# Kernel optimization log

Hardware: AMD Instinct MI355X
Metric: run time of the kernel (lower is better)

The kernel has to match this reference:

```python
import jax, jax.numpy as jnp
import numpy as np


def _gru(x, w_ih, w_hh, b_ih, b_hh):
    # x: [B, T, D]; torch nn.GRU (batch_first) semantics, h0 = 0
    B = x.shape[0]
    H = w_hh.shape[1]
    def step(h, xt):
        gi = xt @ w_ih.T + b_ih          # [B, 3H]
        gh = h @ w_hh.T + b_hh           # [B, 3H]
        ir, iz, inn = jnp.split(gi, 3, axis=-1)
        hr, hz, hn = jnp.split(gh, 3, axis=-1)
        r = jax.nn.sigmoid(ir + hr)
        z = jax.nn.sigmoid(iz + hz)
        n = jnp.tanh(inn + r * hn)
        h_new = (1.0 - z) * n + z * h
        return h_new, h_new
    h0 = jnp.zeros((B, H), x.dtype)
    _, ys = jax.lax.scan(step, h0, jnp.swapaxes(x, 0, 1))
    return jnp.swapaxes(ys, 0, 1)        # [B, T, H]


def setup_inputs() -> dict:
    key = jax.random.key(0)
    ks = iter(jax.random.split(key, 40))
    def p(shape, scale=0.05):
        return jax.random.normal(next(ks), shape, dtype=jnp.float32) * scale
    B, T, Z, S = 1024, 2, 100, 6
    return {
        "x": p((B, T, Z, S), 1.0),
        # actor: GRU(6 -> 64) + SimpleSubActor(64 -> 512 -> 128 -> 1)
        "a_gru_wih": p((192, 6)), "a_gru_whh": p((192, 64)),
        "a_gru_bih": p((192,)), "a_gru_bhh": p((192,)),
        "a_fc1_w": p((512, 64)), "a_fc1_b": p((512,)),
        "a_fc2_w": p((128, 512)), "a_fc2_b": p((128,)),
        "a_fc3_w": p((1, 128)), "a_fc3_b": p((1,)),
        # critic: GRU(35 -> 32) + SimpleSubCritic(32 -> 512 -> 256 -> 1)
        "c_gru_wih": p((96, 35)), "c_gru_whh": p((96, 32)),
        "c_gru_bih": p((96,)), "c_gru_bhh": p((96,)),
        "c_fc1_w": p((512, 32)), "c_fc1_b": p((512,)),
        "c_fc2_w": p((256, 512)), "c_fc2_b": p((256,)),
        "c_fc3_w": p((1, 256)), "c_fc3_b": p((1,)),
        # LocalizedModule(35 -> 512 -> 256 -> 1)
        "lm_fc1_w": p((512, 35)), "lm_fc1_b": p((512,)),
        "lm_fc2_w": p((256, 512)), "lm_fc2_b": p((256,)),
        "lm_fc3_w": p((1, 256)), "lm_fc3_b": p((1,)),
    }


def reference(x, a_gru_wih, a_gru_whh, a_gru_bih, a_gru_bhh,
              a_fc1_w, a_fc1_b, a_fc2_w, a_fc2_b, a_fc3_w, a_fc3_b,
              c_gru_wih, c_gru_whh, c_gru_bih, c_gru_bhh,
              c_fc1_w, c_fc1_b, c_fc2_w, c_fc2_b, c_fc3_w, c_fc3_b,
              lm_fc1_w, lm_fc1_b, lm_fc2_w, lm_fc2_b, lm_fc3_w, lm_fc3_b):
    B, T, Z, S = x.shape
    # ---- SimpleActor: same GRU+MLP shared across zones -> batch zones ----
    # torch: a[i] from x[:, :, i]; torch.stack(a) -> [Z, B, T, 1], then .view(-1, T, Z)
    xz = jnp.transpose(x, (2, 0, 1, 3)).reshape(Z * B, T, S)   # zones-major
    sx = _gru(xz, a_gru_wih, a_gru_whh, a_gru_bih, a_gru_bhh)  # [Z*B, T, 64]
    h = jax.nn.relu(sx @ a_fc1_w.T + a_fc1_b)
    h = jax.nn.relu(h @ a_fc2_w.T + a_fc2_b)
    sa = h @ a_fc3_w.T + a_fc3_b                               # [Z*B, T, 1]
    p = sa.reshape(-1, T, Z)                                   # faithful view(-1, t, nzones)
    # ---- concat action onto state ----
    xc = jnp.concatenate([x, p.reshape(-1, T, Z, 1)], axis=-1)  # [B, T, Z, 7]
    # ---- SimpleCritic: f/q lists reset each iter -> only zone i=99 survives ----
    # neighbors of 99: (99, 89, 100->zeros, 109->zeros, 98)
    zeros = jnp.zeros_like(xc[:, :, Z - 1])
    xi = jnp.concatenate([xc[:, :, 99], xc[:, :, 89], zeros, zeros, xc[:, :, 98]], axis=2)  # [B, T, 35]
    # LocalizedModule on last timestep
    hf = jax.nn.relu(xi[:, -1, :] @ lm_fc1_w.T + lm_fc1_b)
    hf = jax.nn.relu(hf @ lm_fc2_w.T + lm_fc2_b)
    f = hf @ lm_fc3_w.T + lm_fc3_b                             # [B, 1]
    # critic GRU + SimpleSubCritic (it keeps only last timestep)
    xq = _gru(xi, c_gru_wih, c_gru_whh, c_gru_bih, c_gru_bhh)  # [B, T, 32]
    hq = jax.nn.relu(xq[:, -1, :] @ c_fc1_w.T + c_fc1_b)
    hq = jax.nn.relu(hq @ c_fc2_w.T + c_fc2_b)
    qz = hq @ c_fc3_w.T + c_fc3_b                              # [B, 1]
    q = jnp.sum(f + qz, axis=1)                                # [B]
    return p[:, -1], q.reshape(-1, 1)
```

## Files before the change

### kernel.cpp

```cpp
#include <hip/hip_runtime.h>
#include <hip/hip_bf16.h>

#define NB 1024
#define NT 2
#define NZ 100
#define NS 6
#define NSEQ (NZ*NB)

typedef short short8 __attribute__((ext_vector_type(8)));
typedef float floatx4 __attribute__((ext_vector_type(4)));
typedef unsigned int uint2v __attribute__((ext_vector_type(2)));

__device__ __forceinline__ float sigm(float v)     { return 1.0f/(1.0f + __expf(-v)); }
__device__ __forceinline__ float tanhfast(float v) { float t = __expf(2.0f*v); return 1.0f - 2.0f/(t + 1.0f); }
__device__ __forceinline__ unsigned short f2bf(float f) {
    __hip_bfloat16 h = __float2bfloat16(f);
    return *reinterpret_cast<unsigned short*>(&h);
}

#define WS_WIHB   819200
#define WS_WHHB   (WS_WIHB + 192*32*2)
#define WS_W1B    (WS_WHHB + 192*64*2)
#define WS_W2B    (WS_W1B + 512*64*2)
#define WS_L1WB   (WS_W2B + 128*512*2)
#define WS_L2WB   (WS_L1WB + 512*64*2)
#define WS_CF1WB  (WS_L2WB + 256*512*2)
#define WS_CF2WB  (WS_CF1WB + 512*32*2)
#define WS_CWIHB  (WS_CF2WB + 256*512*2)
#define WS_CWHHB  (WS_CWIHB + 96*64*2)

#define PREP_N (116736 + 32768 + 131072 + 16384 + 131072 + 6144 + 3072)

__global__ __launch_bounds__(256)
void prep_kernel(const float* __restrict__ wih, const float* __restrict__ whh,
                 const float* __restrict__ w1,  const float* __restrict__ w2,
                 const float* __restrict__ l1w, const float* __restrict__ l2w,
                 const float* __restrict__ cf1w, const float* __restrict__ cf2w,
                 const float* __restrict__ cwih, const float* __restrict__ cwhh,
                 unsigned short* wihb, unsigned short* whhb,
                 unsigned short* w1b,  unsigned short* w2b,
                 unsigned short* l1wb, unsigned short* l2wb,
                 unsigned short* cf1wb, unsigned short* cf2wb,
                 unsigned short* cwihb, unsigned short* cwhhb)
{
    int e = blockIdx.x*256 + threadIdx.x;
    if (e < 6144) {
        int g = e >> 5, k = e & 31;
        wihb[e] = f2bf(k < 6 ? wih[g*6 + k] : 0.0f);
    } else if (e < 18432) {
        int i = e - 6144;  whhb[i] = f2bf(whh[i]);
    } else if (e < 51200) {
        int i = e - 18432; w1b[i] = f2bf(w1[i]);
    } else if (e < 116736) {
        int i = e - 51200; w2b[i] = f2bf(w2[i]);
    } else if (e < 149504) {
        int i = e - 116736; int o = i >> 6, k = i & 63;
        l1wb[i] = f2bf(k < 35 ? l1w[o*35 + k] : 0.0f);
    } else if (e < 280576) {
        int i = e - 149504; l2wb[i] = f2bf(l2w[i]);
    } else if (e < 296960) {
        int i = e - 280576; cf1wb[i] = f2bf(cf1w[i]);
    } else if (e < 428032) {
        int i = e - 296960; cf2wb[i] = f2bf(cf2w[i]);
    } else if (e < 434176) {
        int i = e - 428032; int o = i >> 6, k = i & 63;
        cwihb[i] = f2bf(k < 35 ? cwih[o*35 + k] : 0.0f);
    } else if (e < PREP_N) {
        int i = e - 434176; cwhhb[i] = f2bf(cwhh[i]);
    }
}

__device__ __forceinline__ int swz(int r) { return ((r & 7) << 4) | ((r & 8) << 3); }

__device__ __forceinline__ short8 ldsfrag(const char* base, int rowstride, int r, int k0) {
    int byte = r*rowstride + k0*2;
    byte ^= swz(r);
    return *reinterpret_cast<const short8*>(base + byte);
}

__device__ __forceinline__ short8 ldsfragC(const char* base, int rowstride, int r, int k0) {
    int byte = r*rowstride + k0*2;
    byte ^= ((r & 7) << 4);
    return *reinterpret_cast<const short8*>(base + byte);
}

__device__ __forceinline__ short8 xfrag(const float* __restrict__ xp) {
    float2 a  = *reinterpret_cast<const float2*>(xp);
    float2 b2 = *reinterpret_cast<const float2*>(xp + 2);
    float2 c  = *reinterpret_cast<const float2*>(xp + 4);
    short8 f;
    f[0] = (short)f2bf(a.x);  f[1] = (short)f2bf(a.y);
    f[2] = (short)f2bf(b2.x); f[3] = (short)f2bf(b2.y);
    f[4] = (short)f2bf(c.x);  f[5] = (short)f2bf(c.y);
    f[6] = 0; f[7] = 0;
    return f;
}

__global__ __launch_bounds__(256)
void actor_mfma(const float* __restrict__ x,
                const unsigned short* __restrict__ wihb, const unsigned short* __restrict__ whhb,
                const float* __restrict__ bih, const float* __restrict__ bhh,
                const unsigned short* __restrict__ w1b, const float* __restrict__ b1,
                const unsigned short* __restrict__ w2b, const float* __restrict__ b2,
                const float* __restrict__ w3, const float* __restrict__ b3,
                float* __restrict__ sa, float* __restrict__ out0)
{
    __shared__ __align__(16) char smem[24576];
    char*  sxb  = smem;
    float* fc3p = (float*)smem;
    char*  h1q  = smem + 8192;
    char*  h0b  = smem + 8192;

    const int tid  = threadIdx.x;
    const int wv   = tid >> 6;
    const int lane = tid & 63;
    const int r16  = lane & 15;
    const int g4   = lane >> 4;
    const int ft   = wv;
    const int s0   = blockIdx.x * 32;
    const int zz   = s0 >> 10;
    const int b0   = s0 & 1023;

    const int fb = ft*16 + g4*4;
    const floatx4 bihR = *reinterpret_cast<const floatx4*>(bih + fb);
    const floatx4 bihZ = *reinterpret_cast<const floatx4*>(bih + 64 + fb);
    const floatx4 bihN = *reinterpret_cast<const floatx4*>(bih + 128 + fb);
    const floatx4 bhhR = *reinterpret_cast<const floatx4*>(bhh + fb);
    const floatx4 bhhZ = *reinterpret_cast<const floatx4*>(bhh + 64 + fb);
    const floatx4 bhhN = *reinterpret_cast<const floatx4*>(bhh + 128 + fb);

    floatx4 h0v[2];
    floatx4 g1R[2], g1Z[2], g1N[2];

    {
        const short8 aR = *reinterpret_cast<const short8*>(wihb + ((ft     )*16 + r16)*32 + g4*8);
        const short8 aZ = *reinterpret_cast<const short8*>(wihb + ((ft +  4)*16 + r16)*32 + g4*8);
        const short8 aN = *reinterpret_cast<const short8*>(wihb + ((ft +  8)*16 + r16)*32 + g4*8);
        #pragma unroll
        for (int u = 0; u < 2; ++u) {
            const int seq = u*16 + r16;
            const float* xrow = x + (((b0 + seq)*NT)*NZ + zz)*NS;
            short8 bx0 = xfrag(xrow);
            short8 bx1 = xfrag(xrow + NZ*NS);
            floatx4 gR = {0,0,0,0}, gZ = {0,0,0,0}, gN = {0,0,0,0};
            gR = __builtin_amdgcn_mfma_f32_16x16x32_bf16(aR, bx0, gR, 0, 0, 0);
            gZ = __builtin_amdgcn_mfma_f32_16x16x32_bf16(aZ, bx0, gZ, 0, 0, 0);
            gN = __builtin_amdgcn_mfma_f32_16x16x32_bf16(aN, bx0, gN, 0, 0, 0);
            floatx4 tR = {0,0,0,0}, tZ = {0,0,0,0}, tN = {0,0,0,0};
            tR = __builtin_amdgcn_mfma_f32_16x16x32_bf16(aR, bx1, tR, 0, 0, 0);
            tZ = __builtin_amdgcn_mfma_f32_16x16x32_bf16(aZ, bx1, tZ, 0, 0, 0);
            tN = __builtin_amdgcn_mfma_f32_16x16x32_bf16(aN, bx1, tN, 0, 0, 0);
            g1R[u] = tR; g1Z[u] = tZ; g1N[u] = tN;
            floatx4 hh;
            #pragma unroll
            for (int q = 0; q < 4; ++q) {
                float r = sigm(gR[q] + bihR[q] + bhhR[q]);
                float z = sigm(gZ[q] + bihZ[q] + bhhZ[q]);
                float n = tanhfast(gN[q] + bihN[q] + r*bhhN[q]);
                hh[q] = (1.0f - z)*n;
            }
            h0v[u] = hh;
            unsigned int lo = (unsigned int)f2bf(hh[0]) | ((unsigned int)f2bf(hh[1]) << 16);
            unsigned int hi = (unsigned int)f2bf(hh[2]) | ((unsigned int)f2bf(hh[3]) << 16);
            uint2v vv = {lo, hi};
            int ba = seq*128 + fb*2; ba ^= swz(seq);
            *reinterpret_cast<uint2v*>(h0b + ba) = vv;
            *reinterpret_cast<uint2v*>(sxb + ba) = vv;
        }
    }
    __syncthreads();

    {
        const short8 wR0 = *reinterpret_cast<const short8*>(whhb + ((ft     )*16 + r16)*64 + g4*8);
        const short8 wR1 = *reinterpret_cast<const short8*>(whhb + ((ft     )*16 + r16)*64 + 32 + g4*8);
        const short8 wZ0 = *reinterpret_cast<const short8*>(whhb + ((ft +  4)*16 + r16)*64 + g4*8);
        const short8 wZ1 = *reinterpret_cast<const short8*>(whhb + ((ft +  4)*16 + r16)*64 + 32 + g4*8);
        const short8 wN0 = *reinterpret_cast<const short8*>(whhb + ((ft +  8)*16 + r16)*64 + g4*8);
        const short8 wN1 = *reinterpret_cast<const short8*>(whhb + ((ft +  8)*16 + r16)*64 + 32 + g4*8);
        #pragma unroll
        for (int u = 0; u < 2; ++u) {
            const int seq = u*16 + r16;
            short8 bh0 = ldsfrag(h0b, 128, seq, g4*8);
            short8 bh1 = ldsfrag(h0b, 128, seq, 32 + g4*8);
            floatx4 hR = {0,0,0,0}, hZ = {0,0,0,0}, hN = {0,0,0,0};
            hR = __builtin_amdgcn_mfma_f32_16x16x32_bf16(wR0, bh0, hR, 0, 0, 0);
            hZ = __builtin_amdgcn_mfma_f32_16x16x32_bf16(wZ0, bh0, hZ, 0, 0, 0);
            hN = __builtin_amdgcn_mfma_f32_16x16x32_bf16(wN0, bh0, hN, 0, 0, 0);
            hR = __builtin_amdgcn_mfma_f32_16x16x32_bf16(wR1, bh1, hR, 0, 0, 0);
            hZ = __builtin_amdgcn_mfma_f32_16x16x32_bf16(wZ1, bh1, hZ, 0, 0, 0);
            hN = __builtin_amdgcn_mfma_f32_16x16x32_bf16(wN1, bh1, hN, 0, 0, 0);
            floatx4 hn;
            #pragma unroll
            for (int q = 0; q < 4; ++q) {
                float r = sigm(g1R[u][q] + bihR[q] + hR[q] + bhhR[q]);
                float z = sigm(g1Z[u][q] + bihZ[q] + hZ[q] + bhhZ[q]);
                float n = tanhfast(g1N[u][q] + bihN[q] + r*(hN[q] + bhhN[q]));
                hn[q] = (1.0f - z)*n + z*h0v[u][q];
            }
            unsigned int lo = (unsigned int)f2bf(hn[0]) | ((unsigned int)f2bf(hn[1]) << 16);
            unsigned int hi = (unsigned int)f2bf(hn[2]) | ((unsigned int)f2bf(hn[3]) << 16);
            uint2v vv = {lo, hi};
            int row = 32 + seq;
            int ba = row*128 + fb*2; ba ^= swz(row);
            *reinterpret_cast<uint2v*>(sxb + ba) = vv;
        }
    }
    __syncthreads();

    const int mt0 = wv*2, mt1 = wv*2 + 1;
    floatx4 acc[2][4];
    {
        const floatx4 bA = *reinterpret_cast<const floatx4*>(b2 + mt0*16 + g4*4);
        const floatx4 bB = *reinterpret_cast<const floatx4*>(b2 + mt1*16 + g4*4);
        #pragma unroll
        for (int rt = 0; rt < 4; ++rt) { acc[0][rt] = bA; acc[1][rt] = bB; }
    }

    #pragma unroll
    for (int qq = 0; qq < 4; ++qq) {
        #pragma unroll
        for (int rt = 0; rt < 4; ++rt) {
            short8 f0 = ldsfrag(sxb, 128, rt*16 + r16, g4*8);
            short8 f1 = ldsfrag(sxb, 128, rt*16 + r16, 32 + g4*8);
            #pragma unroll
            for (int j = 0; j < 2; ++j) {
                int mtg = qq*8 + wv*2 + j;
                int mtl = wv*2 + j;
                const short8 a0 = *reinterpret_cast<const short8*>(w1b + (mtg*16 + r16)*64 + g4*8);
                const short8 a1 = *reinterpret_cast<const short8*>(w1b + (mtg*16 + r16)*64 + 32 + g4*8);
                floatx4 a = *reinterpret_cast<const floatx4*>(b1 + mtg*16 + g4*4);
                a = __builtin_amdgcn_mfma_f32_16x16x32_bf16(a0, f0, a, 0, 0, 0);
                a = __builtin_amdgcn_mfma_f32_16x16x32_bf16(a1, f1, a, 0, 0, 0);
                unsigned int lo = (unsigned int)f2bf(fmaxf(a[0],0.f)) | ((unsigned int)f2bf(fmaxf(a[1],0.f)) << 16);
                unsigned int hi = (unsigned int)f2bf(fmaxf(a[2],0.f)) | ((unsigned int)f2bf(fmaxf(a[3],0.f)) << 16);
                int row = rt*16 + r16;
                int byte = row*256 + (mtl*16 + g4*4)*2; byte ^= swz(row);
                uint2v vv = {lo, hi};
                *reinterpret_cast<uint2v*>(h1q + byte) = vv;
            }
        }
        __syncthreads();

        {
            const unsigned short* wp0 = w2b + (mt0*16 + r16)*512 + qq*128 + g4*8;
            const unsigned short* wp1 = w2b + (mt1*16 + r16)*512 + qq*128 + g4*8;
            #pragma unroll
            for (int ks = 0; ks < 4; ++ks) {
                const short8 a0 = *reinterpret_cast<const short8*>(wp0 + ks*32);
                const short8 a1 = *reinterpret_cast<const short8*>(wp1 + ks*32);
                #pragma unroll
                for (int rt = 0; rt < 4; ++rt) {
                    short8 bb = ldsfrag(h1q, 256, rt*16 + r16, ks*32 + g4*8);
                    acc[0][rt] = __builtin_amdgcn_mfma_f32_16x16x32_bf16(a0, bb, acc[0][rt], 0, 0, 0);
                    acc[1][rt] = __builtin_amdgcn_mfma_f32_16x16x32_bf16(a1, bb, acc[1][rt], 0, 0, 0);
                }
            }
        }
        __syncthreads();
    }

    {
        const floatx4 w3a = *reinterpret_cast<const floatx4*>(w3 + mt0*16 + g4*4);
        const floatx4 w3b = *reinterpret_cast<const floatx4*>(w3 + mt1*16 + g4*4);
        #pragma unroll
        for (int rt = 0; rt < 4; ++rt) {
            float p = fmaxf(acc[0][rt][0],0.f)*w3a[0] + fmaxf(acc[0][rt][1],0.f)*w3a[1]
                    + fmaxf(acc[0][rt][2],0.f)*w3a[2] + fmaxf(acc[0][rt][3],0.f)*w3a[3]
                    + fmaxf(acc[1][rt][0],0.f)*w3b[0] + fmaxf(acc[1][rt][1],0.f)*w3b[1]
                    + fmaxf(acc[1][rt][2],0.f)*w3b[2] + fmaxf(acc[1][rt][3],0.f)*w3b[3];
            p += __shfl_xor(p, 16);
            p += __shfl_xor(p, 32);
            if (g4 == 0) fc3p[wv*64 + rt*16 + r16] = p;
        }
    }
    __syncthreads();

    if (tid < 64) {
        float v = b3[0];
        #pragma unroll
        for (int w = 0; w < 4; ++w) v += fc3p[w*64 + tid];
        int t = tid >> 5, sl = tid & 31;
        int gseq = s0 + sl;
        int i = gseq*2 + t;
        sa[i] = v;
        int m = i % 200;
        if (m >= 100) out0[(i/200)*NZ + (m - 100)] = v;
    }
}

__global__ __launch_bounds__(512)
void critic_mfma(const float* __restrict__ x, const float* __restrict__ sa,
                 const unsigned short* __restrict__ cwihb, const unsigned short* __restrict__ cwhhb,
                 const float* __restrict__ cbih, const float* __restrict__ cbhh,
                 const unsigned short* __restrict__ cf1wb, const float* __restrict__ cf1b,
                 const unsigned short* __restrict__ cf2wb, const float* __restrict__ cf2b,
                 const float* __restrict__ cf3w, const float* __restrict__ cf3b,
                 const unsigned short* __restrict__ l1wb, const float* __restrict__ l1b,
                 const unsigned short* __restrict__ l2wb, const float* __restrict__ l2b,
                 const float* __restrict__ l3w, const float* __restrict__ l3b,
                 float* __restrict__ outq)
{
    __shared__ __align__(16) char smem[25600];
    char*  xib = smem;
    char*  h1b = smem + 4096;
    char*  h0b = smem + 20480;
    char*  hqb = smem + 22528;
    float* fp  = (float*)(smem + 24576);
    float* qp  = (float*)(smem + 25088);

    const int tid  = threadIdx.x;
    const int wv   = tid >> 6;
    const int lane = tid & 63;
    const int r16  = lane & 15;
    const int g4   = lane >> 4;
    const int b0   = blockIdx.x * 16;

    for (int e = tid; e < 2048; e += 512) {
        int trow = e >> 6, k = e & 63;
        int t = trow >> 4, row = trow & 15;
        int b = b0 + row;
        float v = 0.0f;
        if (k < 35) {
            int slot = k / 7, s = k - slot*7;
            int nb = (slot==0)?99:((slot==1)?89:((slot==4)?98:-1));
            if (nb >= 0) v = (s < 6) ? x[((b*NT + t)*NZ + nb)*NS + s]
                                     : sa[b*200 + t*100 + nb];
        }
        int byte = trow*128 + k*2; byte ^= ((trow & 7) << 4);
        *reinterpret_cast<unsigned short*>(xib + byte) = f2bf(v);
    }
    __syncthreads();

    {
        short8 bx0 = ldsfragC(xib, 128, 16 + r16, g4*8);
        short8 bx1 = ldsfragC(xib, 128, 16 + r16, 32 + g4*8);
        #pragma unroll
        for (int j = 0; j < 4; ++j) {
            int mt = wv*4 + j;
            const short8 a0 = *reinterpret_cast<const short8*>(l1wb + (mt*16 + r16)*64 + g4*8);
            const short8 a1 = *reinterpret_cast<const short8*>(l1wb + (mt*16 + r16)*64 + 32 + g4*8);
            floatx4 acc = *reinterpret_cast<const floatx4*>(l1b + mt*16 + g4*4);
            acc = __builtin_amdgcn_mfma_f32_16x16x32_bf16(a0, bx0, acc, 0, 0, 0);
            acc = __builtin_amdgcn_mfma_f32_16x16x32_bf16(a1, bx1, acc, 0, 0, 0);
            unsigned int lo = (unsigned int)f2bf(fmaxf(acc[0],0.f)) | ((unsigned int)f2bf(fmaxf(acc[1],0.f)) << 16);
            unsigned int hi = (unsigned int)f2bf(fmaxf(acc[2],0.f)) | ((unsigned int)f2bf(fmaxf(acc[3],0.f)) << 16);
            int byte = r16*1024 + (mt*16 + g4*4)*2; byte ^= ((r16 & 7) << 4);
            uint2v vv = {lo, hi};
            *reinterpret_cast<uint2v*>(h1b + byte) = vv;
        }
    }
    __syncthreads();

    {
        int mt0 = wv*2, mt1 = wv*2 + 1;
        floatx4 acc0 = *reinterpret_cast<const floatx4*>(l2b + mt0*16 + g4*4);
        floatx4 acc1 = *reinterpret_cast<const floatx4*>(l2b + mt1*16 + g4*4);
        const unsigned short* wp0 = l2wb + (mt0*16 + r16)*512 + g4*8;
        const unsigned short* wp1 = l2wb + (mt1*16 + r16)*512 + g4*8;
        for (int ks = 0; ks < 16; ++ks) {
            short8 bb = ldsfragC(h1b, 1024, r16, ks*32 + g4*8);
            const short8 a0 = *reinterpret_cast<const short8*>(wp0 + ks*32);
            const short8 a1 = *reinterpret_cast<const short8*>(wp1 + ks*32);
            acc0 = __builtin_amdgcn_mfma_f32_16x16x32_bf16(a0, bb, acc0, 0, 0, 0);
            acc1 = __builtin_amdgcn_mfma_f32_16x16x32_bf16(a1, bb, acc1, 0, 0, 0);
        }
        const floatx4 w0 = *reinterpret_cast<const floatx4*>(l3w + mt0*16 + g4*4);
        const floatx4 w1 = *reinterpret_cast<const floatx4*>(l3w + mt1*16 + g4*4);
        float p = fmaxf(acc0[0],0.f)*w0[0] + fmaxf(acc0[1],0.f)*w0[1]
                + fmaxf(acc0[2],0.f)*w0[2] + fmaxf(acc0[3],0.f)*w0[3]
                + fmaxf(acc1[0],0.f)*w1[0] + fmaxf(acc1[1],0.f)*w1[1]
                + fmaxf(acc1[2],0.f)*w1[2] + fmaxf(acc1[3],0.f)*w1[3];
        p += __shfl_xor(p, 16);
        p += __shfl_xor(p, 32);
        if (g4 == 0) fp[wv*16 + r16] = p;
    }
    __syncthreads();

    floatx4 h0r = {0,0,0,0};
    floatx4 gR1 = {0,0,0,0}, gZ1 = {0,0,0,0}, gN1 = {0,0,0,0};
    floatx4 bihR, bihZ, bihN, bhhR, bhhZ, bhhN;
    if (wv < 2) {
        const int hf = wv;
        const int fb = hf*16 + g4*4;
        bihR = *reinterpret_cast<const floatx4*>(cbih + fb);
        bihZ = *reinterpret_cast<const floatx4*>(cbih + 32 + fb);
        bihN = *reinterpret_cast<const floatx4*>(cbih + 64 + fb);
        bhhR = *reinterpret_cast<const floatx4*>(cbhh + fb);
        bhhZ = *reinterpret_cast<const floatx4*>(cbhh + 32 + fb);
        bhhN = *reinterpret_cast<const floatx4*>(cbhh + 64 + fb);
        short8 bx0 = ldsfragC(xib, 128, r16, g4*8);
        short8 bx1 = ldsfragC(xib, 128, r16, 32 + g4*8);
        short8 cx0 = ldsfragC(xib, 128, 16 + r16, g4*8);
        short8 cx1 = ldsfragC(xib, 128, 16 + r16, 32 + g4*8);
        floatx4 gR0 = {0,0,0,0}, gZ0 = {0,0,0,0}, gN0 = {0,0,0,0};
        #pragma unroll
        for (int p = 0; p < 2; ++p) {
            const short8 aR = *reinterpret_cast<const short8*>(cwihb + ((hf    )*16 + r16)*64 + p*32 + g4*8);
            const short8 aZ = *reinterpret_cast<const short8*>(cwihb + ((2+hf  )*16 + r16)*64 + p*32 + g4*8);
            const short8 aN = *reinterpret_cast<const short8*>(cwihb + ((4+hf  )*16 + r16)*64 + p*32 + g4*8);
            short8 b0f = p ? bx1 : bx0;
            short8 b1f = p ? cx1 : cx0;
            gR0 = __builtin_amdgcn_mfma_f32_16x16x32_bf16(aR, b0f, gR0, 0, 0, 0);
            gZ0 = __builtin_amdgcn_mfma_f32_16x16x32_bf16(aZ, b0f, gZ0, 0, 0, 0);
            gN0 = __builtin_amdgcn_mfma_f32_16x16x32_bf16(aN, b0f, gN0, 0, 0, 0);
            gR1 = __builtin_amdgcn_mfma_f32_16x16x32_bf16(aR, b1f, gR1, 0, 0, 0);
            gZ1 = __builtin_amdgcn_mfma_f32_16x16x32_bf16(aZ, b1f, gZ1, 0, 0, 0);
            gN1 = __builtin_amdgcn_mfma_f32_16x16x32_bf16(aN, b1f, gN1, 0, 0, 0);
        }
        #pragma unroll
        for (int q = 0; q < 4; ++q) {
            float r = sigm(gR0[q] + bihR[q] + bhhR[q]);
            float z = sigm(gZ0[q] + bihZ[q] + bhhZ[q]);
            float n = tanhfast(gN0[q] + bihN[q] + r*bhhN[q]);
            h0r[q] = (1.0f - z)*n;
        }
        unsigned int lo = (unsigned int)f2bf(h0r[0]) | ((unsigned int)f2bf(h0r[1]) << 16);
        unsigned int hi = (unsigned int)f2bf(h0r[2]) | ((unsigned int)f2bf(h0r[3]) << 16);
        uint2v vv = {lo, hi};
        int byte = r16*128 + fb*2; byte ^= ((r16 & 7) << 4);
        *reinterpret_cast<uint2v*>(h0b + byte) = vv;
    }
    __syncthreads();
    if (wv < 2) {
        const int hf = wv;
        const int fb = hf*16 + g4*4;
        short8 bh = ldsfragC(h0b, 128, r16, g4*8);
        const short8 aR = *reinterpret_cast<const short8*>(cwhhb + ((hf    )*16 + r16)*32 + g4*8);
        const short8 aZ = *reinterpret_cast<const short8*>(cwhhb + ((2+hf  )*16 + r16)*32 + g4*8);
        const short8 aN = *reinterpret_cast<const short8*>(cwhhb + ((4+hf  )*16 + r16)*32 + g4*8);
        floatx4 hR = {0,0,0,0}, hZ = {0,0,0,0}, hN = {0,0,0,0};
        hR = __builtin_amdgcn_mfma_f32_16x16x32_bf16(aR, bh, hR, 0, 0, 0);
        hZ = __builtin_amdgcn_mfma_f32_16x16x32_bf16(aZ, bh, hZ, 0, 0, 0);
        hN = __builtin_amdgcn_mfma_f32_16x16x32_bf16(aN, bh, hN, 0, 0, 0);
        floatx4 hn;
        #pragma unroll
        for (int q = 0; q < 4; ++q) {
            float r = sigm(gR1[q] + bihR[q] + hR[q] + bhhR[q]);
            float z = sigm(gZ1[q] + bihZ[q] + hZ[q] + bhhZ[q]);
            float n = tanhfast(gN1[q] + bihN[q] + r*(hN[q] + bhhN[q]));
            hn[q] = (1.0f - z)*n + z*h0r[q];
        }
        unsigned int lo = (unsigned int)f2bf(hn[0]) | ((unsigned int)f2bf(hn[1]) << 16);
        unsigned int hi = (unsigned int)f2bf(hn[2]) | ((unsigned int)f2bf(hn[3]) << 16);
        uint2v vv = {lo, hi};
        int byte = r16*128 + fb*2; byte ^= ((r16 & 7) << 4);
        *reinterpret_cast<uint2v*>(hqb + byte) = vv;
    }
    __syncthreads();

    {
        short8 bq = ldsfragC(hqb, 128, r16, g4*8);
        #pragma unroll
        for (int j = 0; j < 4; ++j) {
            int mt = wv*4 + j;
            const short8 a = *reinterpret_cast<const short8*>(cf1wb + (mt*16 + r16)*32 + g4*8);
            floatx4 acc = *reinterpret_cast<const floatx4*>(cf1b + mt*16 + g4*4);
            acc = __builtin_amdgcn_mfma_f32_16x16x32_bf16(a, bq, acc, 0, 0, 0);
            unsigned int lo = (unsigned int)f2bf(fmaxf(acc[0],0.f)) | ((unsigned int)f2bf(fmaxf(acc[1],0.f)) << 16);
            unsigned int hi = (unsigned int)f2bf(fmaxf(acc[2],0.f)) | ((unsigned int)f2bf(fmaxf(acc[3],0.f)) << 16);
            int byte = r16*1024 + (mt*16 + g4*4)*2; byte ^= ((r16 & 7) << 4);
            uint2v vv = {lo, hi};
            *reinterpret_cast<uint2v*>(h1b + byte) = vv;
        }
    }
    __syncthreads();

    {
        int mt0 = wv*2, mt1 = wv*2 + 1;
        floatx4 acc0 = *reinterpret_cast<const floatx4*>(cf2b + mt0*16 + g4*4);
        floatx4 acc1 = *reinterpret_cast<const floatx4*>(cf2b + mt1*16 + g4*4);
        const unsigned short* wp0 = cf2wb + (mt0*16 + r16)*512 + g4*8;
        const unsigned short* wp1 = cf2wb + (mt1*16 + r16)*512 + g4*8;
        for (int ks = 0; ks < 16; ++ks) {
            short8 bb = ldsfragC(h1b, 1024, r16, ks*32 + g4*8);
            const short8 a0 = *reinterpret_cast<const short8*>(wp0 + ks*32);
            const short8 a1 = *reinterpret_cast<const short8*>(wp1 + ks*32);
            acc0 = __builtin_amdgcn_mfma_f32_16x16x32_bf16(a0, bb, acc0, 0, 0, 0);
            acc1 = __builtin_amdgcn_mfma_f32_16x16x32_bf16(a1, bb, acc1, 0, 0, 0);
        }
        const floatx4 w0 = *reinterpret_cast<const floatx4*>(cf3w + mt0*16 + g4*4);
        const floatx4 w1 = *reinterpret_cast<const floatx4*>(cf3w + mt1*16 + g4*4);
        float p = fmaxf(acc0[0],0.f)*w0[0] + fmaxf(acc0[1],0.f)*w0[1]
                + fmaxf(acc0[2],0.f)*w0[2] + fmaxf(acc0[3],0.f)*w0[3]
                + fmaxf(acc1[0],0.f)*w1[0] + fmaxf(acc1[1],0.f)*w1[1]
                + fmaxf(acc1[2],0.f)*w1[2] + fmaxf(acc1[3],0.f)*w1[3];
        p += __shfl_xor(p, 16);
        p += __shfl_xor(p, 32);
        if (g4 == 0) qp[wv*16 + r16] = p;
    }
    __syncthreads();

    if (tid < 16) {
        float f = l3b[0], qz = cf3b[0];
        #pragma unroll
        for (int w = 0; w < 8; ++w) { f += fp[w*16 + tid]; qz += qp[w*16 + tid]; }
        outq[b0 + tid] = f + qz;
    }
}

extern "C" void kernel_launch(void* const* d_in, const int* in_sizes, int n_in,
                              void* d_out, int out_size, void* d_ws, size_t ws_size,
                              hipStream_t stream)
{
    (void)in_sizes; (void)n_in; (void)out_size; (void)ws_size;
    const float* x     = (const float*)d_in[0];
    const float* a_wih = (const float*)d_in[1];
    const float* a_whh = (const float*)d_in[2];
    const float* a_bih = (const float*)d_in[3];
    const float* a_bhh = (const float*)d_in[4];
    const float* a1w   = (const float*)d_in[5];
    const float* a1b   = (const float*)d_in[6];
    const float* a2w   = (const float*)d_in[7];
    const float* a2b   = (const float*)d_in[8];
    const float* a3w   = (const float*)d_in[9];
    const float* a3b   = (const float*)d_in[10];
    const float* cwih  = (const float*)d_in[11];
    const float* cwhh  = (const float*)d_in[12];
    const float* cbih  = (const float*)d_in[13];
    const float* cbhh  = (const float*)d_in[14];
    const float* cf1w  = (const float*)d_in[15];
    const float* cf1b  = (const float*)d_in[16];
    const float* cf2w  = (const float*)d_in[17];
    const float* cf2b  = (const float*)d_in[18];
    const float* cf3w  = (const float*)d_in[19];
    const float* cf3b  = (const float*)d_in[20];
    const float* l1w   = (const float*)d_in[21];
    const float* l1b   = (const float*)d_in[22];
    const float* l2w   = (const float*)d_in[23];
    const float* l2b   = (const float*)d_in[24];
    const float* l3w   = (const float*)d_in[25];
    const float* l3b   = (const float*)d_in[26];

    float* sa = (float*)d_ws;
    unsigned short* wihb  = (unsigned short*)((char*)d_ws + WS_WIHB);
    unsigned short* whhb  = (unsigned short*)((char*)d_ws + WS_WHHB);
    unsigned short* w1b   = (unsigned short*)((char*)d_ws + WS_W1B);
    unsigned short* w2b   = (unsigned short*)((char*)d_ws + WS_W2B);
    unsigned short* l1wb  = (unsigned short*)((char*)d_ws + WS_L1WB);
    unsigned short* l2wb  = (unsigned short*)((char*)d_ws + WS_L2WB);
    unsigned short* cf1wb = (unsigned short*)((char*)d_ws + WS_CF1WB);
    unsigned short* cf2wb = (unsigned short*)((char*)d_ws + WS_CF2WB);
    unsigned short* cwihb = (unsigned short*)((char*)d_ws + WS_CWIHB);
    unsigned short* cwhhb = (unsigned short*)((char*)d_ws + WS_CWHHB);
    float* out0 = (float*)d_out;
    float* outq = (float*)d_out + NB*NZ;

    hipLaunchKernelGGL(prep_kernel, dim3((PREP_N + 255)/256), dim3(256), 0, stream,
                       a_wih, a_whh, a1w, a2w, l1w, l2w, cf1w, cf2w, cwih, cwhh,
                       wihb, whhb, w1b, w2b, l1wb, l2wb, cf1wb, cf2wb, cwihb, cwhhb);
    hipLaunchKernelGGL(actor_mfma, dim3(NSEQ/32), dim3(256), 0, stream,
                       x, wihb, whhb, a_bih, a_bhh, w1b, a1b, w2b, a2b, a3w, a3b, sa, out0);
    hipLaunchKernelGGL(critic_mfma, dim3(NB/16), dim3(512), 0, stream,
                       x, sa, cwihb, cwhhb, cbih, cbhh, cf1wb, cf1b, cf2wb, cf2b, cf3w, cf3b,
                       l1wb, l1b, l2wb, l2b, l3w, l3b, outq);
}
```

Measured before the change: 153.0 us.

## Process actor fc1/fc2 in two 256-wide chunks and hoist LDS input fragments

The actor MLP's hidden layer was processed in four 128-wide chunks, each needing its own barrier. It now uses two 256-wide chunks in a larger shared buffer, which halves the barriers and drops the last one. The GRU-output fragments are loaded from shared memory once into registers instead of once per chunk. The redundant copy of h0 is removed by reading it from the shared sequence buffer, and the swizzle is simplified to one variant. In exchange, the kernel uses more shared memory and registers, which may lower occupancy.

```diff
diff --git a/kernel.cpp b/kernel.cpp
--- a/kernel.cpp
+++ b/kernel.cpp
@@ -70,17 +70,11 @@
     }
 }
 
-__device__ __forceinline__ int swz(int r) { return ((r & 7) << 4) | ((r & 8) << 3); }
+__device__ __forceinline__ int swz(int r) { return (r & 7) << 4; }
 
 __device__ __forceinline__ short8 ldsfrag(const char* base, int rowstride, int r, int k0) {
     int byte = r*rowstride + k0*2;
     byte ^= swz(r);
-    return *reinterpret_cast<const short8*>(base + byte);
-}
-
-__device__ __forceinline__ short8 ldsfragC(const char* base, int rowstride, int r, int k0) {
-    int byte = r*rowstride + k0*2;
-    byte ^= ((r & 7) << 4);
     return *reinterpret_cast<const short8*>(base + byte);
 }
 
@@ -105,11 +99,10 @@
                 const float* __restrict__ w3, const float* __restrict__ b3,
                 float* __restrict__ sa, float* __restrict__ out0)
 {
-    __shared__ __align__(16) char smem[24576];
+    __shared__ __align__(16) char smem[40960];
     char*  sxb  = smem;
     float* fc3p = (float*)smem;
-    char*  h1q  = smem + 8192;
-    char*  h0b  = smem + 8192;
+    char*  h1b  = smem + 8192;
 
     const int tid  = threadIdx.x;
     const int wv   = tid >> 6;
@@ -164,7 +157,6 @@
             unsigned int hi = (unsigned int)f2bf(hh[2]) | ((unsigned int)f2bf(hh[3]) << 16);
             uint2v vv = {lo, hi};
             int ba = seq*128 + fb*2; ba ^= swz(seq);
-            *reinterpret_cast<uint2v*>(h0b + ba) = vv;
             *reinterpret_cast<uint2v*>(sxb + ba) = vv;
         }
     }
@@ -180,8 +172,8 @@
         #pragma unroll
         for (int u = 0; u < 2; ++u) {
             const int seq = u*16 + r16;
-            short8 bh0 = ldsfrag(h0b, 128, seq, g4*8);
-            short8 bh1 = ldsfrag(h0b, 128, seq, 32 + g4*8);
+            short8 bh0 = ldsfrag(sxb, 128, seq, g4*8);
+            short8 bh1 = ldsfrag(sxb, 128, seq, 32 + g4*8);
             floatx4 hR = {0,0,0,0}, hZ = {0,0,0,0}, hN = {0,0,0,0};
             hR = __builtin_amdgcn_mfma_f32_16x16x32_bf16(wR0, bh0, hR, 0, 0, 0);
             hZ = __builtin_amdgcn_mfma_f32_16x16x32_bf16(wZ0, bh0, hZ, 0, 0, 0);
@@ -207,6 +199,13 @@
     }
     __syncthreads();
 
+    short8 fr[4][2];
+    #pragma unroll
+    for (int rt = 0; rt < 4; ++rt) {
+        fr[rt][0] = ldsfrag(sxb, 128, rt*16 + r16, g4*8);
+        fr[rt][1] = ldsfrag(sxb, 128, rt*16 + r16, 32 + g4*8);
+    }
+
     const int mt0 = wv*2, mt1 = wv*2 + 1;
     floatx4 acc[2][4];
     {
@@ -217,46 +216,45 @@
     }
 
     #pragma unroll
-    for (int qq = 0; qq < 4; ++qq) {
-        #pragma unroll
-        for (int rt = 0; rt < 4; ++rt) {
-            short8 f0 = ldsfrag(sxb, 128, rt*16 + r16, g4*8);
-            short8 f1 = ldsfrag(sxb, 128, rt*16 + r16, 32 + g4*8);
+    for (int h = 0; h < 2; ++h) {
+        #pragma unroll
+        for (int j = 0; j < 4; ++j) {
+            int mtg = h*16 + wv*4 + j;
+            int mtl = wv*4 + j;
+            const short8 a0 = *reinterpret_cast<const short8*>(w1b + (mtg*16 + r16)*64 + g4*8);
+            const short8 a1 = *reinterpret_cast<const short8*>(w1b + (mtg*16 + r16)*64 + 32 + g4*8);
+            const floatx4 bias = *reinterpret_cast<const floatx4*>(b1 + mtg*16 + g4*4);
             #pragma unroll
-            for (int j = 0; j < 2; ++j) {
-                int mtg = qq*8 + wv*2 + j;
-                int mtl = wv*2 + j;
-                const short8 a0 = *reinterpret_cast<const short8*>(w1b + (mtg*16 + r16)*64 + g4*8);
-                const short8 a1 = *reinterpret_cast<const short8*>(w1b + (mtg*16 + r16)*64 + 32 + g4*8);
-                floatx4 a = *reinterpret_cast<const floatx4*>(b1 + mtg*16 + g4*4);
-                a = __builtin_amdgcn_mfma_f32_16x16x32_bf16(a0, f0, a, 0, 0, 0);
-                a = __builtin_amdgcn_mfma_f32_16x16x32_bf16(a1, f1, a, 0, 0, 0);
+            for (int rt = 0; rt < 4; ++rt) {
+                floatx4 a = bias;
+                a = __builtin_amdgcn_mfma_f32_16x16x32_bf16(a0, fr[rt][0], a, 0, 0, 0);
+                a = __builtin_amdgcn_mfma_f32_16x16x32_bf16(a1, fr[rt][1], a, 0, 0, 0);
                 unsigned int lo = (unsigned int)f2bf(fmaxf(a[0],0.f)) | ((unsigned int)f2bf(fmaxf(a[1],0.f)) << 16);
                 unsigned int hi = (unsigned int)f2bf(fmaxf(a[2],0.f)) | ((unsigned int)f2bf(fmaxf(a[3],0.f)) << 16);
                 int row = rt*16 + r16;
-                int byte = row*256 + (mtl*16 + g4*4)*2; byte ^= swz(row);
+                int byte = row*512 + (mtl*16 + g4*4)*2; byte ^= swz(row);
                 uint2v vv = {lo, hi};
-                *reinterpret_cast<uint2v*>(h1q + byte) = vv;
+                *reinterpret_cast<uint2v*>(h1b + byte) = vv;
             }
         }
         __syncthreads();
 
         {
-            const unsigned short* wp0 = w2b + (mt0*16 + r16)*512 + qq*128 + g4*8;
-            const unsigned short* wp1 = w2b + (mt1*16 + r16)*512 + qq*128 + g4*8;
+            const unsigned short* wp0 = w2b + (mt0*16 + r16)*512 + h*256 + g4*8;
+            const unsigned short* wp1 = w2b + (mt1*16 + r16)*512 + h*256 + g4*8;
             #pragma unroll
-            for (int ks = 0; ks < 4; ++ks) {
+            for (int ks = 0; ks < 8; ++ks) {
                 const short8 a0 = *reinterpret_cast<const short8*>(wp0 + ks*32);
                 const short8 a1 = *reinterpret_cast<const short8*>(wp1 + ks*32);
                 #pragma unroll
                 for (int rt = 0; rt < 4; ++rt) {
-                    short8 bb = ldsfrag(h1q, 256, rt*16 + r16, ks*32 + g4*8);
+                    short8 bb = ldsfrag(h1b, 512, rt*16 + r16, ks*32 + g4*8);
                     acc[0][rt] = __builtin_amdgcn_mfma_f32_16x16x32_bf16(a0, bb, acc[0][rt], 0, 0, 0);
                     acc[1][rt] = __builtin_amdgcn_mfma_f32_16x16x32_bf16(a1, bb, acc[1][rt], 0, 0, 0);
                 }
             }
         }
-        __syncthreads();
+        if (h == 0) __syncthreads();
     }
 
     {
@@ -332,8 +330,8 @@
     __syncthreads();
 
     {
-        short8 bx0 = ldsfragC(xib, 128, 16 + r16, g4*8);
-        short8 bx1 = ldsfragC(xib, 128, 16 + r16, 32 + g4*8);
+        short8 bx0 = ldsfrag(xib, 128, 16 + r16, g4*8);
+        short8 bx1 = ldsfrag(xib, 128, 16 + r16, 32 + g4*8);
         #pragma unroll
         for (int j = 0; j < 4; ++j) {
             int mt = wv*4 + j;
@@ -358,7 +356,7 @@
         const unsigned short* wp0 = l2wb + (mt0*16 + r16)*512 + g4*8;
         const unsigned short* wp1 = l2wb + (mt1*16 + r16)*512 + g4*8;
         for (int ks = 0; ks < 16; ++ks) {
-            short8 bb = ldsfragC(h1b, 1024, r16, ks*32 + g4*8);
+            short8 bb = ldsfrag(h1b, 1024, r16, ks*32 + g4*8);
             const short8 a0 = *reinterpret_cast<const short8*>(wp0 + ks*32);
             const short8 a1 = *reinterpret_cast<const short8*>(wp1 + ks*32);
             acc0 = __builtin_amdgcn_mfma_f32_16x16x32_bf16(a0, bb, acc0, 0, 0, 0);
@@ -388,10 +386,10 @@
         bhhR = *reinterpret_cast<const floatx4*>(cbhh + fb);
         bhhZ = *reinterpret_cast<const floatx4*>(cbhh + 32 + fb);
         bhhN = *reinterpret_cast<const floatx4*>(cbhh + 64 + fb);
-        short8 bx0 = ldsfragC(xib, 128, r16, g4*8);
-        short8 bx1 = ldsfragC(xib, 128, r16, 32 + g4*8);
-        short8 cx0 = ldsfragC(xib, 128, 16 + r16, g4*8);
-        short8 cx1 = ldsfragC(xib, 128, 16 + r16, 32 + g4*8);
+        short8 bx0 = ldsfrag(xib, 128, r16, g4*8);
+        short8 bx1 = ldsfrag(xib, 128, r16, 32 + g4*8);
+        short8 cx0 = ldsfrag(xib, 128, 16 + r16, g4*8);
+        short8 cx1 = ldsfrag(xib, 128, 16 + r16, 32 + g4*8);
         floatx4 gR0 = {0,0,0,0}, gZ0 = {0,0,0,0}, gN0 = {0,0,0,0};
         #pragma unroll
         for (int p = 0; p < 2; ++p) {
@@ -424,7 +422,7 @@
     if (wv < 2) {
         const int hf = wv;
         const int fb = hf*16 + g4*4;
-        short8 bh = ldsfragC(h0b, 128, r16, g4*8);
+        short8 bh = ldsfrag(h0b, 128, r16, g4*8);
         const short8 aR = *reinterpret_cast<const short8*>(cwhhb + ((hf    )*16 + r16)*32 + g4*8);
         const short8 aZ = *reinterpret_cast<const short8*>(cwhhb + ((2+hf  )*16 + r16)*32 + g4*8);
         const short8 aN = *reinterpret_cast<const short8*>(cwhhb + ((4+hf  )*16 + r16)*32 + g4*8);
@@ -449,7 +447,7 @@
     __syncthreads();
 
     {
-        short8 bq = ldsfragC(hqb, 128, r16, g4*8);
+        short8 bq = ldsfrag(hqb, 128, r16, g4*8);
         #pragma unroll
         for (int j = 0; j < 4; ++j) {
             int mt = wv*4 + j;
@@ -472,7 +470,7 @@
         const unsigned short* wp0 = cf2wb + (mt0*16 + r16)*512 + g4*8;
         const unsigned short* wp1 = cf2wb + (mt1*16 + r16)*512 + g4*8;
         for (int ks = 0; ks < 16; ++ks) {
-            short8 bb = ldsfragC(h1b, 1024, r16, ks*32 + g4*8);
+            short8 bb = ldsfrag(h1b, 1024, r16, ks*32 + g4*8);
             const short8 a0 = *reinterpret_cast<const short8*>(wp0 + ks*32);
             const short8 a1 = *reinterpret_cast<const short8*>(wp1 + ks*32);
             acc0 = __builtin_amdgcn_mfma_f32_16x16x32_bf16(a0, bb, acc0, 0, 0, 0);
```

Measured after the change: 131.9 us (median of 2 runs). -13.8%, faster.
